# Optimization experiments

Measured on AMD Instinct MI355X. Metric: run time of the kernel, lower is better.

## Reference

```python
import jax, jax.numpy as jnp
import numpy as np
from jax import lax

B, C, T = 64, 122, 500
COUT, D, H, FF, L = 64, 128, 8, 256, 2
NSUB, NCLS = 13, 4
EPS = 1e-5


def _gelu(x):
    return jax.nn.gelu(x, approximate=False)  # torch nn.GELU default (erf)


def _bn(x, g, b, m, v):
    # eval-mode BatchNorm1d over channel dim of [N, C, T]
    scale = (g / jnp.sqrt(v + EPS))[None, :, None]
    return (x - m[None, :, None]) * scale + b[None, :, None]


def _ln(x, g, b):
    mu = x.mean(-1, keepdims=True)
    var = ((x - mu) ** 2).mean(-1, keepdims=True)
    return (x - mu) / jnp.sqrt(var + EPS) * g + b


def _conv1d(x, w, b, pad):
    y = lax.conv_general_dilated(x, w, (1,), [(pad, pad)], dimension_numbers=('NCH', 'OIH', 'NCH'))
    return y + b[None, :, None]


def forward(x, subject_ids, conv1_w, conv1_b, bn1_g, bn1_b, bn1_m, bn1_v,
            conv2_w, conv2_b, bn2_g, bn2_b, bn2_m, bn2_v,
            proj_w, proj_b, elec_emb,
            qkv_w, qkv_b, out_w, out_b, ln1_g, ln1_b,
            ff1_w, ff1_b, ff2_w, ff2_b, ln2_g, ln2_b,
            heads_w, heads_b):
    bsz = x.shape[0]
    h = x.reshape(bsz * C, 1, T)                               # [B*C, 1, T]
    h = _gelu(_bn(_conv1d(h, conv1_w, conv1_b, 4), bn1_g, bn1_b, bn1_m, bn1_v))
    h = h.reshape(bsz * C, COUT, T // 2, 2).max(-1)            # MaxPool1d(2)
    h = _gelu(_bn(_conv1d(h, conv2_w, conv2_b, 2), bn2_g, bn2_b, bn2_m, bn2_v))
    h = h.mean(-1)                                             # AdaptiveAvgPool1d(1)
    tok = h @ proj_w.T + proj_b                                # [B*C, D]
    tok = tok.reshape(bsz, C, D) + elec_emb[:, :C, :]
    dh = D // H
    inv_sqrt_dh = 1.0 / float(np.sqrt(dh))
    for l in range(L):  # post-norm TransformerEncoderLayer, gelu activation
        qkv = jnp.einsum('bsd,ed->bse', tok, qkv_w[l]) + qkv_b[l]
        q, k, v = jnp.split(qkv, 3, axis=-1)
        q = q.reshape(bsz, C, H, dh)
        k = k.reshape(bsz, C, H, dh)
        v = v.reshape(bsz, C, H, dh)
        att = jax.nn.softmax(jnp.einsum('bqhd,bkhd->bhqk', q, k) * inv_sqrt_dh, axis=-1)
        ctx = jnp.einsum('bhqk,bkhd->bqhd', att, v).reshape(bsz, C, D)
        tok = _ln(tok + ctx @ out_w[l].T + out_b[l], ln1_g[l], ln1_b[l])
        ff = _gelu(tok @ ff1_w[l].T + ff1_b[l]) @ ff2_w[l].T + ff2_b[l]
        tok = _ln(tok + ff, ln2_g[l], ln2_b[l])
    pooled = tok.mean(axis=1)                                  # [B, D]
    # per-subject head routing == gather subject's weight/bias, batched matvec
    hw = heads_w[subject_ids]                                  # [B, NCLS, D]
    hb = heads_b[subject_ids]                                  # [B, NCLS]
    return jnp.einsum('bd,bcd->bc', pooled, hw) + hb


def setup_inputs() -> dict:
    key = jax.random.key(0)
    ks = jax.random.split(key, 16)
    def n(i, shape, s=0.02):
        return jax.random.normal(ks[i], shape, jnp.float32) * s
    return {
        'x': jax.random.normal(ks[0], (B, C, T), jnp.float32),
        'subject_ids': jax.random.randint(ks[1], (B,), 0, NSUB),
        'conv1_w': n(2, (COUT, 1, 9), 0.3), 'conv1_b': jnp.zeros((COUT,), jnp.float32),
        'bn1_g': jnp.ones((COUT,), jnp.float32), 'bn1_b': jnp.zeros((COUT,), jnp.float32),
        'bn1_m': jnp.zeros((COUT,), jnp.float32), 'bn1_v': jnp.ones((COUT,), jnp.float32),
        'conv2_w': n(3, (COUT, COUT, 5), 0.05), 'conv2_b': jnp.zeros((COUT,), jnp.float32),
        'bn2_g': jnp.ones((COUT,), jnp.float32), 'bn2_b': jnp.zeros((COUT,), jnp.float32),
        'bn2_m': jnp.zeros((COUT,), jnp.float32), 'bn2_v': jnp.ones((COUT,), jnp.float32),
        'proj_w': n(4, (D, COUT), 0.05), 'proj_b': jnp.zeros((D,), jnp.float32),
        'elec_emb': n(5, (1, C, D), 0.02),
        'qkv_w': n(6, (L, 3 * D, D), 0.05), 'qkv_b': jnp.zeros((L, 3 * D), jnp.float32),
        'out_w': n(7, (L, D, D), 0.05), 'out_b': jnp.zeros((L, D), jnp.float32),
        'ln1_g': jnp.ones((L, D), jnp.float32), 'ln1_b': jnp.zeros((L, D), jnp.float32),
        'ff1_w': n(8, (L, FF, D), 0.05), 'ff1_b': jnp.zeros((L, FF), jnp.float32),
        'ff2_w': n(9, (L, D, FF), 0.05), 'ff2_b': jnp.zeros((L, D), jnp.float32),
        'ln2_g': jnp.ones((L, D), jnp.float32), 'ln2_b': jnp.zeros((L, D), jnp.float32),
        'heads_w': n(10, (NSUB, NCLS, D), 0.05), 'heads_b': jnp.zeros((NSUB, NCLS), jnp.float32),
    }


def reference(x, subject_ids, conv1_w, conv1_b, bn1_g, bn1_b, bn1_m, bn1_v,
              conv2_w, conv2_b, bn2_g, bn2_b, bn2_m, bn2_v,
              proj_w, proj_b, elec_emb,
              qkv_w, qkv_b, out_w, out_b, ln1_g, ln1_b,
              ff1_w, ff1_b, ff2_w, ff2_b, ln2_g, ln2_b,
              heads_w, heads_b):
    return forward(x, subject_ids, conv1_w, conv1_b, bn1_g, bn1_b, bn1_m, bn1_v,
                   conv2_w, conv2_b, bn2_g, bn2_b, bn2_m, bn2_v,
                   proj_w, proj_b, elec_emb,
                   qkv_w, qkv_b, out_w, out_b, ln1_g, ln1_b,
                   ff1_w, ff1_b, ff2_w, ff2_b, ln2_g, ln2_b,
                   heads_w, heads_b)
```

## Files before the change

### kernel.cpp

```cpp
#include <hip/hip_runtime.h>
#include <math.h>

#define BB 64
#define CC 122
#define TT 500
#define NCOUT 64
#define DD 128
#define HHEADS 8
#define FFDIM 256
#define NLAYER 2
#define EPS 1e-5f
#define SEQ (BB*CC)

#define WS_W2T     0u
#define WS_S1      20480u
#define WS_SH1     20544u
#define WS_S2      20608u
#define WS_SH2     20672u
#define WS_WBF     20736u
#define WS_TOK     151808u
#define WS_QKVB    1151232u
#define WS_VTB     2150656u
#define WS_GTAB    2674944u
#define WS_W1S     2675968u

#define WB_QKV  0u
#define WB_OUT  98304u
#define WB_FF1  131072u
#define WB_FF2  196608u

typedef __attribute__((ext_vector_type(8))) short bf16x8;
typedef __attribute__((ext_vector_type(4))) float f32x4;

__device__ __forceinline__ unsigned short f2bf(float f) {
    unsigned int u = __float_as_uint(f);
    unsigned int r = u + 0x7FFFu + ((u >> 16) & 1u);
    return (unsigned short)(r >> 16);
}

__device__ __forceinline__ float gelu_fast(float x) {
    float z = fabsf(x) * 0.70710678118654752f;
    float t = __builtin_amdgcn_rcpf(fmaf(0.3275911f, z, 1.0f));
    float p = fmaf(fmaf(fmaf(fmaf(1.061405429f, t, -1.453152027f), t,
                             1.421413741f), t, -0.284496736f), t, 0.254829592f);
    float e = __expf(-z * z);
    float erf_abs = fmaf(-p * t, e, 1.0f);
    float erf_x = copysignf(erf_abs, x);
    return 0.5f * x * (1.0f + erf_x);
}

__device__ __forceinline__ float gelu_tab(float x, const float* __restrict__ gt) {
    float p = fmaf(x, 32.0f, 256.0f);
    p = fminf(fmaxf(p, 0.0f), 511.999f);
    int i = (int)p;
    float fr = p - (float)i;
    float2 gd = *(const float2*)&gt[2*i];
    return fmaf(fr, gd.y, gd.x);
}

__global__ void prep_kernel(const float* __restrict__ conv1_w, const float* __restrict__ conv1_b,
                            const float* __restrict__ bn1_g, const float* __restrict__ bn1_b,
                            const float* __restrict__ bn1_m, const float* __restrict__ bn1_v,
                            const float* __restrict__ conv2_w, const float* __restrict__ conv2_b,
                            const float* __restrict__ bn2_g, const float* __restrict__ bn2_b,
                            const float* __restrict__ bn2_m, const float* __restrict__ bn2_v,
                            const float* __restrict__ qkv_w, const float* __restrict__ out_w,
                            const float* __restrict__ ff1_w, const float* __restrict__ ff2_w,
                            float* __restrict__ ws) {
    int idx = blockIdx.x * blockDim.x + threadIdx.x;
    if (idx < 20480) {
        int ci = idx & 63; int co = (idx >> 6) & 63; int kk = idx >> 12;
        unsigned short* wt = (unsigned short*)(ws + WS_W2T);
        wt[idx] = f2bf(conv2_w[(co*64 + ci)*5 + kk]);
    } else if (idx < 20544) {
        int i = idx - 20480;
        float s = bn1_g[i] * rsqrtf(bn1_v[i] + EPS);
        ws[WS_S1 + i] = s;
        ws[WS_SH1 + i] = (conv1_b[i] - bn1_m[i]) * s + bn1_b[i];
    } else if (idx < 20608) {
        int i = idx - 20544;
        float s = bn2_g[i] * rsqrtf(bn2_v[i] + EPS);
        ws[WS_S2 + i] = s;
        ws[WS_SH2 + i] = (conv2_b[i] - bn2_m[i]) * s + bn2_b[i];
    } else if (idx < 282752) {
        int r = idx - 20608;
        unsigned short* wbf = (unsigned short*)(ws + WS_WBF);
        float v;
        if (r < 98304)       v = qkv_w[r];
        else if (r < 131072) v = out_w[r - 98304];
        else if (r < 196608) v = ff1_w[r - 131072];
        else                 v = ff2_w[r - 196608];
        wbf[r] = f2bf(v);
    } else if (idx < 283264) {
        int i = idx - 282752;
        float x0 = (i - 256) * 0.03125f;
        float x1 = x0 + 0.03125f;
        float g0 = 0.5f*x0*(1.0f + erff(x0*0.70710678118654752f));
        float g1 = 0.5f*x1*(1.0f + erff(x1*0.70710678118654752f));
        ws[WS_GTAB + 2*i]     = g0;
        ws[WS_GTAB + 2*i + 1] = g1 - g0;
    } else if (idx < 285312) {
        int i = idx - 283264;
        int co = i >> 5, k = i & 31;
        unsigned short* w1s = (unsigned short*)(ws + WS_W1S);
        float s = bn1_g[co] * rsqrtf(bn1_v[co] + EPS);
        w1s[i] = (k < 9) ? f2bf(conv1_w[co*9 + k] * s) : (unsigned short)0;
    }
}

__global__ __launch_bounds__(256, 4) void conv_kernel(const float* __restrict__ x,
            const float* __restrict__ proj_w, const float* __restrict__ proj_b,
            const float* __restrict__ elec,
            const float* __restrict__ wsr, float* __restrict__ tok) {
    __shared__ __align__(16) unsigned short h1s[264*64];
    __shared__ __align__(16) unsigned short xbf[544];
    __shared__ __align__(16) float gtab[1024];
    __shared__ float part[256];
    __shared__ float mean_l[64];
    int n = blockIdx.x;
    int c = n % CC;
    int tid = threadIdx.x;
    const float* xg = x + (size_t)n * TT;

    for (int i = tid; i < 544; i += 256) {
        unsigned short v = 0;
        if (i >= 4 && i < 504) v = f2bf(xg[i-4]);
        xbf[i] = v;
    }
    {
        const float4* gsrc = (const float4*)(wsr + WS_GTAB);
        float4* gdst = (float4*)gtab;
        if (tid < 256) gdst[tid] = gsrc[tid];
    }
    for (int idx = tid; idx < 14*64; idx += 256) {
        int rr = idx >> 6;
        int r = (rr < 2) ? rr : (rr - 2 + 252);
        h1s[r*64 + (idx & 63)] = 0;
    }
    __syncthreads();

    int lane = tid & 63;
    int w = tid >> 6;
    int ln15 = lane & 15, lg = lane >> 4;

    {
        const unsigned short* w1s = (const unsigned short*)(wsr + WS_W1S);
        bf16x8 b1f[4];
        float sh1v[4];
#pragma unroll
        for (int nt = 0; nt < 4; nt++) {
            int co = nt*16 + ln15;
            b1f[nt] = *(const bf16x8*)&w1s[co*32 + lg*8];
            sh1v[nt] = wsr[WS_SH1 + co];
        }
        for (int mi = 0; mi < 8; mi++) {
            int mt = w*8 + mi;
            int t = mt*16 + ln15;
            short e[8];
#pragma unroll
            for (int j = 0; j < 8; j++) e[j] = (short)xbf[t + lg*8 + j];
            bf16x8 af = {e[0],e[1],e[2],e[3],e[4],e[5],e[6],e[7]};
#pragma unroll
            for (int nt = 0; nt < 4; nt++) {
                f32x4 cacc = __builtin_amdgcn_mfma_f32_16x16x32_bf16(af, b1f[nt],
                                (f32x4){0.f,0.f,0.f,0.f}, 0, 0, 0);
                float g0 = gelu_tab(cacc[0] + sh1v[nt], gtab);
                float g1 = gelu_tab(cacc[1] + sh1v[nt], gtab);
                float g2 = gelu_tab(cacc[2] + sh1v[nt], gtab);
                float g3 = gelu_tab(cacc[3] + sh1v[nt], gtab);
                int tpA = mt*8 + lg*2;
                if (tpA < 250) {
                    int co = nt*16 + ln15;
                    int r = tpA + 2;
                    int cp = (co >> 3) ^ (r & 7);
                    h1s[r*64 + cp*8 + (co & 7)] = f2bf(fmaxf(g0, g1));
                    int r2 = r + 1;
                    int cp2 = (co >> 3) ^ (r2 & 7);
                    h1s[r2*64 + cp2*8 + (co & 7)] = f2bf(fmaxf(g2, g3));
                }
            }
        }
    }
    __syncthreads();

    const unsigned short* wt = (const unsigned short*)(wsr + WS_W2T);
    f32x4 acc[4][4];
#pragma unroll
    for (int mi = 0; mi < 4; mi++)
#pragma unroll
        for (int nt = 0; nt < 4; nt++) acc[mi][nt] = (f32x4){0.f, 0.f, 0.f, 0.f};

    const unsigned short* wbase = wt + ln15*64 + lg*8;
#pragma unroll
    for (int kk = 0; kk < 5; kk++) {
#pragma unroll
        for (int s = 0; s < 2; s++) {
            bf16x8 bfv[4];
#pragma unroll
            for (int nt = 0; nt < 4; nt++)
                bfv[nt] = *(const bf16x8*)(wbase + kk*4096 + nt*1024 + s*32);
#pragma unroll
            for (int mi = 0; mi < 4; mi++) {
                int r = (w*4 + mi)*16 + ln15 + kk;
                int cp = (s*4 + lg) ^ (r & 7);
                bf16x8 af = *(const bf16x8*)&h1s[r*64 + cp*8];
#pragma unroll
                for (int nt = 0; nt < 4; nt++)
                    acc[mi][nt] = __builtin_amdgcn_mfma_f32_16x16x32_bf16(af, bfv[nt], acc[mi][nt], 0, 0, 0);
            }
        }
    }

#pragma unroll
    for (int nt = 0; nt < 4; nt++) {
        int co2 = nt*16 + ln15;
        float sc = wsr[WS_S2 + co2], sh = wsr[WS_SH2 + co2];
        float p = 0.f;
#pragma unroll
        for (int mi = 0; mi < 4; mi++) {
            int tbase = (w*4 + mi)*16 + lg*4;
#pragma unroll
            for (int i = 0; i < 4; i++) {
                if (tbase + i < 250)
                    p += gelu_tab(fmaf(acc[mi][nt][i], sc, sh), gtab);
            }
        }
        p += __shfl_down(p, 32, 64);
        p += __shfl_down(p, 16, 64);
        if (lane < 16) part[w*64 + co2] = p;
    }
    __syncthreads();
    if (tid < 64) {
        mean_l[tid] = (part[tid] + part[64+tid] + part[128+tid] + part[192+tid]) * (1.0f/250.0f);
    }
    __syncthreads();

    if (tid < DD) {
        int d = tid;
        float a = proj_b[d] + elec[c*DD + d];
#pragma unroll 8
        for (int o = 0; o < 64; o++) a = fmaf(mean_l[o], proj_w[d*64 + o], a);
        tok[(size_t)n * DD + d] = a;
    }
}

__global__ __launch_bounds__(256) void qkv_gemm(const float* __restrict__ Aptr,
        const unsigned short* __restrict__ Bbf,
        const float* __restrict__ bias,
        unsigned short* __restrict__ qkvb,
        unsigned short* __restrict__ vtb) {
    const int tid = threadIdx.x;
    const int m0 = blockIdx.x * 32;
    const int y  = blockIdx.y;
    const int n0 = y * 128;
    __shared__ __align__(16) unsigned short As[32*128];

    const float* A = Aptr + (size_t)m0 * 128;
    for (int i = tid; i < 1024; i += 256) {
        int m = i >> 5; int kq = (i & 31)*4;
        float4 v = *(const float4*)(A + m*128 + kq);
        int cp = (kq >> 3) ^ (m & 15);
        short4 s4 = make_short4((short)f2bf(v.x), (short)f2bf(v.y),
                                (short)f2bf(v.z), (short)f2bf(v.w));
        *(short4*)&As[m*128 + cp*8 + (kq & 7)] = s4;
    }
    __syncthreads();

    const int lane = tid & 63, w = tid >> 6;
    const int ln15 = lane & 15, lg = lane >> 4;
    f32x4 acc[2][2];
#pragma unroll
    for (int mi = 0; mi < 2; mi++)
#pragma unroll
        for (int ni = 0; ni < 2; ni++) acc[mi][ni] = (f32x4){0.f, 0.f, 0.f, 0.f};

    const unsigned short* Bb = Bbf + (size_t)n0 * 128;
#pragma unroll
    for (int kt = 0; kt < 4; kt++) {
        bf16x8 af[2], bfv[2];
#pragma unroll
        for (int mi = 0; mi < 2; mi++) {
            int m = mi*16 + ln15;
            int cp = (kt*4 + lg) ^ (m & 15);
            af[mi] = *(const bf16x8*)&As[m*128 + cp*8];
        }
#pragma unroll
        for (int ni = 0; ni < 2; ni++) {
            int nn = (w*2 + ni)*16 + ln15;
            bfv[ni] = *(const bf16x8*)&Bb[(size_t)nn*128 + kt*32 + lg*8];
        }
#pragma unroll
        for (int mi = 0; mi < 2; mi++)
#pragma unroll
            for (int ni = 0; ni < 2; ni++)
                acc[mi][ni] = __builtin_amdgcn_mfma_f32_16x16x32_bf16(af[mi], bfv[ni], acc[mi][ni], 0, 0, 0);
    }

#pragma unroll
    for (int mi = 0; mi < 2; mi++)
#pragma unroll
        for (int ni = 0; ni < 2; ni++) {
            int nloc = (w*2 + ni)*16 + ln15;
            float bb = bias[n0 + nloc];
#pragma unroll
            for (int i = 0; i < 4; i++) {
                int ml = mi*16 + lg*4 + i;
                int nrow = m0 + ml;
                unsigned short us = f2bf(acc[mi][ni][i] + bb);
                if (y < 2) {
                    qkvb[(size_t)nrow*256 + n0 + nloc] = us;
                } else {
                    int bq = nrow / 122;
                    int j  = nrow - bq*122;
                    vtb[((size_t)(bq*128 + nloc))*128 + j] = us;
                }
            }
        }
}

__global__ __launch_bounds__(256) void attn_tail(
        const unsigned short* __restrict__ qkvb,
        const unsigned short* __restrict__ vtb,
        const unsigned short* __restrict__ outW, const float* __restrict__ outb,
        float* __restrict__ tok,
        const float* __restrict__ ln1g, const float* __restrict__ ln1b,
        const unsigned short* __restrict__ B1, const float* __restrict__ b1,
        const unsigned short* __restrict__ B2, const float* __restrict__ b2,
        const float* __restrict__ ln2g, const float* __restrict__ ln2b) {
    __shared__ float Cs[32*129];
    __shared__ __align__(16) unsigned short Pregion[4*32*128];
    __shared__ __align__(16) unsigned short ctxs[32*128];

    const int tid = threadIdx.x;
    const int blk = blockIdx.x;
    const int b = blk >> 2, mq = blk & 3;
    const int m0l = mq * 32;
    const int lane = tid & 63, w = tid >> 6;
    const int ln15 = lane & 15, lg = lane >> 4;

    const unsigned short* qb = qkvb + (size_t)b * 122 * 256;
    unsigned short* Pw = Pregion + w * 4096;

#pragma unroll
    for (int hs = 0; hs < 2; hs++) {
        int h = w + hs*4;
        bf16x8 af[2];
#pragma unroll
        for (int mi = 0; mi < 2; mi++) {
            int mrow = m0l + mi*16 + ln15;
            int gr = (mrow < 122) ? mrow : 121;
            bf16x8 z = {0,0,0,0,0,0,0,0};
            if (lg < 2) z = *(const bf16x8*)(qb + gr*256 + h*16 + lg*8);
            af[mi] = z;
        }
        f32x4 S[2][8];
#pragma unroll
        for (int nt = 0; nt < 8; nt++) {
            int j = nt*16 + ln15;
            int gj = (j < 122) ? j : 121;
            bf16x8 bv = {0,0,0,0,0,0,0,0};
            if (lg < 2) bv = *(const bf16x8*)(qb + gj*256 + 128 + h*16 + lg*8);
#pragma unroll
            for (int mi = 0; mi < 2; mi++)
                S[mi][nt] = __builtin_amdgcn_mfma_f32_16x16x32_bf16(af[mi], bv,
                                (f32x4){0.f,0.f,0.f,0.f}, 0, 0, 0);
        }
        float sm[2][4];
#pragma unroll
        for (int mi = 0; mi < 2; mi++)
#pragma unroll
            for (int i = 0; i < 4; i++) {
                float m_ = -1e30f;
#pragma unroll
                for (int nt = 0; nt < 8; nt++) {
                    float v = S[mi][nt][i] * 0.25f;
                    if (nt == 7 && ln15 >= 10) v = -1e30f;
                    S[mi][nt][i] = v;
                    m_ = fmaxf(m_, v);
                }
                m_ = fmaxf(m_, __shfl_xor(m_, 1, 64));
                m_ = fmaxf(m_, __shfl_xor(m_, 2, 64));
                m_ = fmaxf(m_, __shfl_xor(m_, 4, 64));
                m_ = fmaxf(m_, __shfl_xor(m_, 8, 64));
                float s_ = 0.f;
#pragma unroll
                for (int nt = 0; nt < 8; nt++) {
                    float e = __expf(S[mi][nt][i] - m_);
                    S[mi][nt][i] = e;
                    s_ += e;
                }
                s_ += __shfl_xor(s_, 1, 64);
                s_ += __shfl_xor(s_, 2, 64);
                s_ += __shfl_xor(s_, 4, 64);
                s_ += __shfl_xor(s_, 8, 64);
                sm[mi][i] = s_;
            }
#pragma unroll
        for (int mi = 0; mi < 2; mi++)
#pragma unroll
            for (int nt = 0; nt < 8; nt++)
#pragma unroll
                for (int i = 0; i < 4; i++) {
                    int rp = mi*16 + lg*4 + i;
                    int j = nt*16 + ln15;
                    int cp = (j >> 3) ^ (rp & 15);
                    Pw[rp*128 + cp*8 + (j & 7)] = f2bf(S[mi][nt][i]);
                }
        f32x4 cacc[2] = {(f32x4){0.f,0.f,0.f,0.f}, (f32x4){0.f,0.f,0.f,0.f}};
#pragma unroll
        for (int kt = 0; kt < 4; kt++) {
            bf16x8 bv = *(const bf16x8*)(vtb + ((size_t)(b*128 + h*16 + ln15))*128 + kt*32 + lg*8);
#pragma unroll
            for (int mi = 0; mi < 2; mi++) {
                int m = mi*16 + ln15;
                int cp = (kt*4 + lg) ^ (m & 15);
                bf16x8 ap = *(const bf16x8*)&Pw[m*128 + cp*8];
                cacc[mi] = __builtin_amdgcn_mfma_f32_16x16x32_bf16(ap, bv, cacc[mi], 0, 0, 0);
            }
        }
#pragma unroll
        for (int mi = 0; mi < 2; mi++)
#pragma unroll
            for (int i = 0; i < 4; i++) {
                float inv = __builtin_amdgcn_rcpf(sm[mi][i]);
                int rp = mi*16 + lg*4 + i;
                int ccol = h*16 + ln15;
                int cp = (ccol >> 3) ^ (rp & 15);
                ctxs[rp*128 + cp*8 + (ccol & 7)] = f2bf(cacc[mi][i] * inv);
            }
    }
    __syncthreads();

    {
        f32x4 acc[2][2];
#pragma unroll
        for (int mi = 0; mi < 2; mi++)
#pragma unroll
            for (int ni = 0; ni < 2; ni++) acc[mi][ni] = (f32x4){0.f,0.f,0.f,0.f};
#pragma unroll
        for (int kt = 0; kt < 4; kt++) {
            bf16x8 afm[2], bv[2];
#pragma unroll
            for (int mi = 0; mi < 2; mi++) {
                int m = mi*16 + ln15;
                int cp = (kt*4 + lg) ^ (m & 15);
                afm[mi] = *(const bf16x8*)&ctxs[m*128 + cp*8];
            }
#pragma unroll
            for (int ni = 0; ni < 2; ni++) {
                int nn = (w*2 + ni)*16 + ln15;
                bv[ni] = *(const bf16x8*)&outW[(size_t)nn*128 + kt*32 + lg*8];
            }
#pragma unroll
            for (int mi = 0; mi < 2; mi++)
#pragma unroll
                for (int ni = 0; ni < 2; ni++)
                    acc[mi][ni] = __builtin_amdgcn_mfma_f32_16x16x32_bf16(afm[mi], bv[ni], acc[mi][ni], 0, 0, 0);
        }
#pragma unroll
        for (int mi = 0; mi < 2; mi++)
#pragma unroll
            for (int ni = 0; ni < 2; ni++) {
                int nloc = (w*2 + ni)*16 + ln15;
                float bb = outb[nloc];
#pragma unroll
                for (int i = 0; i < 4; i++) {
                    int ml = mi*16 + lg*4 + i;
                    int mrow = m0l + ml;
                    int grow = b*122 + ((mrow < 122) ? mrow : 121);
                    Cs[ml*129 + nloc] = acc[mi][ni][i] + bb + tok[(size_t)grow*128 + nloc];
                }
            }
    }
    __syncthreads();

    unsigned short* ln1buf = Pregion;
    unsigned short* Hs = Pregion + 4096;
    {
        int r = tid >> 3, sub = tid & 7;
        float s1 = 0.f, s2 = 0.f;
#pragma unroll
        for (int j = 0; j < 16; j++) {
            float vv = Cs[r*129 + sub*16 + j];
            s1 += vv; s2 += vv*vv;
        }
        s1 += __shfl_down(s1, 4, 64); s2 += __shfl_down(s2, 4, 64);
        s1 += __shfl_down(s1, 2, 64); s2 += __shfl_down(s2, 2, 64);
        s1 += __shfl_down(s1, 1, 64); s2 += __shfl_down(s2, 1, 64);
        int lb = lane & 56;
        s1 = __shfl(s1, lb, 64); s2 = __shfl(s2, lb, 64);
        float mu = s1 * (1.0f/128.0f);
        float var = s2 * (1.0f/128.0f) - mu*mu;
        float rstd = rsqrtf(var + EPS);
#pragma unroll
        for (int j = 0; j < 16; j++) {
            int nloc = sub*16 + j;
            float vv = (Cs[r*129 + nloc] - mu) * rstd * ln1g[nloc] + ln1b[nloc];
            Cs[r*129 + nloc] = vv;
            int cp = (nloc >> 3) ^ (r & 15);
            ln1buf[r*128 + cp*8 + (nloc & 7)] = f2bf(vv);
        }
    }
    __syncthreads();

    {
        f32x4 acc1[2][4];
#pragma unroll
        for (int mi = 0; mi < 2; mi++)
#pragma unroll
            for (int ni = 0; ni < 4; ni++) acc1[mi][ni] = (f32x4){0.f,0.f,0.f,0.f};
#pragma unroll
        for (int kt = 0; kt < 4; kt++) {
            bf16x8 afm[2];
#pragma unroll
            for (int mi = 0; mi < 2; mi++) {
                int m = mi*16 + ln15;
                int cp = (kt*4 + lg) ^ (m & 15);
                afm[mi] = *(const bf16x8*)&ln1buf[m*128 + cp*8];
            }
#pragma unroll
            for (int ni = 0; ni < 4; ni++) {
                int nn = w*64 + ni*16 + ln15;
                bf16x8 bv = *(const bf16x8*)&B1[(size_t)nn*128 + kt*32 + lg*8];
#pragma unroll
                for (int mi = 0; mi < 2; mi++)
                    acc1[mi][ni] = __builtin_amdgcn_mfma_f32_16x16x32_bf16(afm[mi], bv, acc1[mi][ni], 0, 0, 0);
            }
        }
#pragma unroll
        for (int ni = 0; ni < 4; ni++) {
            int nn = w*64 + ni*16 + ln15;
            float bb = b1[nn];
#pragma unroll
            for (int mi = 0; mi < 2; mi++)
#pragma unroll
                for (int i = 0; i < 4; i++) {
                    int m = mi*16 + lg*4 + i;
                    float v = gelu_fast(acc1[mi][ni][i] + bb);
                    int cp = (nn >> 3) ^ (m & 15);
                    Hs[m*256 + cp*8 + (nn & 7)] = f2bf(v);
                }
        }
    }
    __syncthreads();

    {
        f32x4 acc2[2][2];
#pragma unroll
        for (int mi = 0; mi < 2; mi++)
#pragma unroll
            for (int ni = 0; ni < 2; ni++) acc2[mi][ni] = (f32x4){0.f,0.f,0.f,0.f};
#pragma unroll
        for (int kt = 0; kt < 8; kt++) {
            bf16x8 afm[2];
#pragma unroll
            for (int mi = 0; mi < 2; mi++) {
                int m = mi*16 + ln15;
                int cp = (kt*4 + lg) ^ (m & 15);
                afm[mi] = *(const bf16x8*)&Hs[m*256 + cp*8];
            }
#pragma unroll
            for (int ni = 0; ni < 2; ni++) {
                int nn = (w*2 + ni)*16 + ln15;
                bf16x8 bv = *(const bf16x8*)&B2[(size_t)nn*256 + kt*32 + lg*8];
#pragma unroll
                for (int mi = 0; mi < 2; mi++)
                    acc2[mi][ni] = __builtin_amdgcn_mfma_f32_16x16x32_bf16(afm[mi], bv, acc2[mi][ni], 0, 0, 0);
            }
        }
#pragma unroll
        for (int mi = 0; mi < 2; mi++)
#pragma unroll
            for (int ni = 0; ni < 2; ni++) {
                int nloc = (w*2 + ni)*16 + ln15;
                float bb = b2[nloc];
#pragma unroll
                for (int i = 0; i < 4; i++) {
                    int ml = mi*16 + lg*4 + i;
                    Cs[ml*129 + nloc] = acc2[mi][ni][i] + bb + Cs[ml*129 + nloc];
                }
            }
    }
    __syncthreads();

    {
        int r = tid >> 3, sub = tid & 7;
        float s1 = 0.f, s2 = 0.f;
#pragma unroll
        for (int j = 0; j < 16; j++) {
            float vv = Cs[r*129 + sub*16 + j];
            s1 += vv; s2 += vv*vv;
        }
        s1 += __shfl_down(s1, 4, 64); s2 += __shfl_down(s2, 4, 64);
        s1 += __shfl_down(s1, 2, 64); s2 += __shfl_down(s2, 2, 64);
        s1 += __shfl_down(s1, 1, 64); s2 += __shfl_down(s2, 1, 64);
        int lb = lane & 56;
        s1 = __shfl(s1, lb, 64); s2 = __shfl(s2, lb, 64);
        float mu = s1 * (1.0f/128.0f);
        float var = s2 * (1.0f/128.0f) - mu*mu;
        float rstd = rsqrtf(var + EPS);
        if (m0l + r < 122) {
#pragma unroll
            for (int j = 0; j < 16; j++) {
                int nloc = sub*16 + j;
                float vv = (Cs[r*129 + nloc] - mu) * rstd * ln2g[nloc] + ln2b[nloc];
                tok[((size_t)(b*122 + m0l + r))*128 + nloc] = vv;
            }
        }
    }
}

__global__ __launch_bounds__(128) void final_kernel(const float* __restrict__ tok,
        const int* __restrict__ sid,
        const float* __restrict__ hw, const float* __restrict__ hb,
        float* __restrict__ outp) {
    __shared__ float pool[DD];
    int b = blockIdx.x, tid = threadIdx.x;
    float s = 0.f;
    for (int c2 = 0; c2 < CC; c2++) s += tok[((size_t)b*CC + c2)*DD + tid];
    pool[tid] = s * (1.0f/(float)CC);
    __syncthreads();
    if (tid < 4) {
        int sb = sid[b];
        const float* w = hw + ((size_t)sb*4 + tid)*DD;
        float a = hb[sb*4 + tid];
#pragma unroll 8
        for (int d = 0; d < DD; d++) a = fmaf(pool[d], w[d], a);
        outp[b*4 + tid] = a;
    }
}

extern "C" void kernel_launch(void* const* d_in, const int* in_sizes, int n_in,
                              void* d_out, int out_size, void* d_ws, size_t ws_size,
                              hipStream_t stream) {
    const float* x       = (const float*)d_in[0];
    const int*   sid     = (const int*)  d_in[1];
    const float* conv1_w = (const float*)d_in[2];
    const float* conv1_b = (const float*)d_in[3];
    const float* bn1_g   = (const float*)d_in[4];
    const float* bn1_b   = (const float*)d_in[5];
    const float* bn1_m   = (const float*)d_in[6];
    const float* bn1_v   = (const float*)d_in[7];
    const float* conv2_w = (const float*)d_in[8];
    const float* conv2_b = (const float*)d_in[9];
    const float* bn2_g   = (const float*)d_in[10];
    const float* bn2_b   = (const float*)d_in[11];
    const float* bn2_m   = (const float*)d_in[12];
    const float* bn2_v   = (const float*)d_in[13];
    const float* proj_w  = (const float*)d_in[14];
    const float* proj_b  = (const float*)d_in[15];
    const float* elec    = (const float*)d_in[16];
    const float* qkv_w   = (const float*)d_in[17];
    const float* qkv_b   = (const float*)d_in[18];
    const float* out_w   = (const float*)d_in[19];
    const float* out_b   = (const float*)d_in[20];
    const float* ln1_g   = (const float*)d_in[21];
    const float* ln1_b   = (const float*)d_in[22];
    const float* ff1_w   = (const float*)d_in[23];
    const float* ff1_b   = (const float*)d_in[24];
    const float* ff2_w   = (const float*)d_in[25];
    const float* ff2_b   = (const float*)d_in[26];
    const float* ln2_g   = (const float*)d_in[27];
    const float* ln2_b   = (const float*)d_in[28];
    const float* heads_w = (const float*)d_in[29];
    const float* heads_b = (const float*)d_in[30];
    float* ws = (float*)d_ws;
    const unsigned short* wbf = (const unsigned short*)(ws + WS_WBF);
    unsigned short* qkvb = (unsigned short*)(ws + WS_QKVB);
    unsigned short* vtb  = (unsigned short*)(ws + WS_VTB);

    prep_kernel<<<(285312 + 255)/256, 256, 0, stream>>>(
        conv1_w, conv1_b, bn1_g, bn1_b, bn1_m, bn1_v,
        conv2_w, conv2_b, bn2_g, bn2_b, bn2_m, bn2_v,
        qkv_w, out_w, ff1_w, ff2_w, ws);

    conv_kernel<<<SEQ, 256, 0, stream>>>(x, proj_w, proj_b, elec, ws, ws + WS_TOK);

    for (int l = 0; l < NLAYER; l++) {
        qkv_gemm<<<dim3(244,3), 256, 0, stream>>>(
            ws + WS_TOK, wbf + WB_QKV + l*49152, qkv_b + l*384, qkvb, vtb);
        attn_tail<<<BB*4, 256, 0, stream>>>(
            qkvb, vtb,
            wbf + WB_OUT + l*16384, out_b + l*128,
            ws + WS_TOK, ln1_g + l*128, ln1_b + l*128,
            wbf + WB_FF1 + l*32768, ff1_b + l*256,
            wbf + WB_FF2 + l*32768, ff2_b + l*128,
            ln2_g + l*128, ln2_b + l*128);
    }

    final_kernel<<<BB, 128, 0, stream>>>(ws + WS_TOK, sid, heads_w, heads_b, (float*)d_out);
}
```

Baseline: 434.5 us.

## Double attn_tail block to 512 threads, one wave per head

The attention/FFN tail kernel goes from 4 to 8 waves per block. Each wave now handles one head instead of two, and the out-proj, FF1, FF2 and layernorm phases are re-split across 8 waves with smaller per-wave tiles. The aim is more latency hiding and more parallel work, since the grid has only 256 blocks. In exchange, the per-wave P buffer shrinks to 16 rows, so each wave processes its two 16-row M tiles one after the other, and there are more barrier participants.

```diff
diff --git a/kernel.cpp b/kernel.cpp
--- a/kernel.cpp
+++ b/kernel.cpp
@@ -318,7 +318,7 @@
         }
 }
 
-__global__ __launch_bounds__(256) void attn_tail(
+__global__ __launch_bounds__(512) void attn_tail(
         const unsigned short* __restrict__ qkvb,
         const unsigned short* __restrict__ vtb,
         const unsigned short* __restrict__ outW, const float* __restrict__ outb,
@@ -328,7 +328,7 @@
         const unsigned short* __restrict__ B2, const float* __restrict__ b2,
         const float* __restrict__ ln2g, const float* __restrict__ ln2b) {
     __shared__ float Cs[32*129];
-    __shared__ __align__(16) unsigned short Pregion[4*32*128];
+    __shared__ __align__(16) unsigned short Pregion[8*16*128];
     __shared__ __align__(16) unsigned short ctxs[32*128];
 
     const int tid = threadIdx.x;
@@ -339,43 +339,35 @@
     const int ln15 = lane & 15, lg = lane >> 4;
 
     const unsigned short* qb = qkvb + (size_t)b * 122 * 256;
-    unsigned short* Pw = Pregion + w * 4096;
-
-#pragma unroll
-    for (int hs = 0; hs < 2; hs++) {
-        int h = w + hs*4;
-        bf16x8 af[2];
-#pragma unroll
-        for (int mi = 0; mi < 2; mi++) {
-            int mrow = m0l + mi*16 + ln15;
+    unsigned short* Pw = Pregion + w * 2048;
+
+    {
+        const int h = w;
+#pragma unroll
+        for (int mt = 0; mt < 2; mt++) {
+            int mrow = m0l + mt*16 + ln15;
             int gr = (mrow < 122) ? mrow : 121;
-            bf16x8 z = {0,0,0,0,0,0,0,0};
-            if (lg < 2) z = *(const bf16x8*)(qb + gr*256 + h*16 + lg*8);
-            af[mi] = z;
-        }
-        f32x4 S[2][8];
-#pragma unroll
-        for (int nt = 0; nt < 8; nt++) {
-            int j = nt*16 + ln15;
-            int gj = (j < 122) ? j : 121;
-            bf16x8 bv = {0,0,0,0,0,0,0,0};
-            if (lg < 2) bv = *(const bf16x8*)(qb + gj*256 + 128 + h*16 + lg*8);
-#pragma unroll
-            for (int mi = 0; mi < 2; mi++)
-                S[mi][nt] = __builtin_amdgcn_mfma_f32_16x16x32_bf16(af[mi], bv,
-                                (f32x4){0.f,0.f,0.f,0.f}, 0, 0, 0);
-        }
-        float sm[2][4];
-#pragma unroll
-        for (int mi = 0; mi < 2; mi++)
+            bf16x8 af = {0,0,0,0,0,0,0,0};
+            if (lg < 2) af = *(const bf16x8*)(qb + gr*256 + h*16 + lg*8);
+            f32x4 S[8];
+#pragma unroll
+            for (int nt = 0; nt < 8; nt++) {
+                int j = nt*16 + ln15;
+                int gj = (j < 122) ? j : 121;
+                bf16x8 bv = {0,0,0,0,0,0,0,0};
+                if (lg < 2) bv = *(const bf16x8*)(qb + gj*256 + 128 + h*16 + lg*8);
+                S[nt] = __builtin_amdgcn_mfma_f32_16x16x32_bf16(af, bv,
+                            (f32x4){0.f,0.f,0.f,0.f}, 0, 0, 0);
+            }
+            float sm[4];
 #pragma unroll
             for (int i = 0; i < 4; i++) {
                 float m_ = -1e30f;
 #pragma unroll
                 for (int nt = 0; nt < 8; nt++) {
-                    float v = S[mi][nt][i] * 0.25f;
+                    float v = S[nt][i] * 0.25f;
                     if (nt == 7 && ln15 >= 10) v = -1e30f;
-                    S[mi][nt][i] = v;
+                    S[nt][i] = v;
                     m_ = fmaxf(m_, v);
                 }
                 m_ = fmaxf(m_, __shfl_xor(m_, 1, 64));
@@ -385,91 +377,71 @@
                 float s_ = 0.f;
 #pragma unroll
                 for (int nt = 0; nt < 8; nt++) {
-                    float e = __expf(S[mi][nt][i] - m_);
-                    S[mi][nt][i] = e;
+                    float e = __expf(S[nt][i] - m_);
+                    S[nt][i] = e;
                     s_ += e;
                 }
                 s_ += __shfl_xor(s_, 1, 64);
                 s_ += __shfl_xor(s_, 2, 64);
                 s_ += __shfl_xor(s_, 4, 64);
                 s_ += __shfl_xor(s_, 8, 64);
-                sm[mi][i] = s_;
-            }
-#pragma unroll
-        for (int mi = 0; mi < 2; mi++)
+                sm[i] = s_;
+            }
 #pragma unroll
             for (int nt = 0; nt < 8; nt++)
 #pragma unroll
                 for (int i = 0; i < 4; i++) {
-                    int rp = mi*16 + lg*4 + i;
+                    int rp = lg*4 + i;
                     int j = nt*16 + ln15;
-                    int cp = (j >> 3) ^ (rp & 15);
-                    Pw[rp*128 + cp*8 + (j & 7)] = f2bf(S[mi][nt][i]);
+                    int cp = (j >> 3) ^ rp;
+                    Pw[rp*128 + cp*8 + (j & 7)] = f2bf(S[nt][i]);
                 }
-        f32x4 cacc[2] = {(f32x4){0.f,0.f,0.f,0.f}, (f32x4){0.f,0.f,0.f,0.f}};
+            f32x4 cacc = (f32x4){0.f,0.f,0.f,0.f};
+#pragma unroll
+            for (int kt = 0; kt < 4; kt++) {
+                bf16x8 bv = *(const bf16x8*)(vtb + ((size_t)(b*128 + h*16 + ln15))*128 + kt*32 + lg*8);
+                int m = ln15;
+                int cp = (kt*4 + lg) ^ m;
+                bf16x8 ap = *(const bf16x8*)&Pw[m*128 + cp*8];
+                cacc = __builtin_amdgcn_mfma_f32_16x16x32_bf16(ap, bv, cacc, 0, 0, 0);
+            }
+#pragma unroll
+            for (int i = 0; i < 4; i++) {
+                float inv = __builtin_amdgcn_rcpf(sm[i]);
+                int rp = mt*16 + lg*4 + i;
+                int ccol = h*16 + ln15;
+                int cp = (ccol >> 3) ^ (rp & 15);
+                ctxs[rp*128 + cp*8 + (ccol & 7)] = f2bf(cacc[i] * inv);
+            }
+        }
+    }
+    __syncthreads();
+
+    {
+        f32x4 acc[2];
+#pragma unroll
+        for (int mi = 0; mi < 2; mi++) acc[mi] = (f32x4){0.f,0.f,0.f,0.f};
+        int nn = w*16 + ln15;
 #pragma unroll
         for (int kt = 0; kt < 4; kt++) {
-            bf16x8 bv = *(const bf16x8*)(vtb + ((size_t)(b*128 + h*16 + ln15))*128 + kt*32 + lg*8);
+            bf16x8 bv = *(const bf16x8*)&outW[(size_t)nn*128 + kt*32 + lg*8];
 #pragma unroll
             for (int mi = 0; mi < 2; mi++) {
                 int m = mi*16 + ln15;
                 int cp = (kt*4 + lg) ^ (m & 15);
-                bf16x8 ap = *(const bf16x8*)&Pw[m*128 + cp*8];
-                cacc[mi] = __builtin_amdgcn_mfma_f32_16x16x32_bf16(ap, bv, cacc[mi], 0, 0, 0);
-            }
-        }
+                bf16x8 afm = *(const bf16x8*)&ctxs[m*128 + cp*8];
+                acc[mi] = __builtin_amdgcn_mfma_f32_16x16x32_bf16(afm, bv, acc[mi], 0, 0, 0);
+            }
+        }
+        float bb = outb[nn];
 #pragma unroll
         for (int mi = 0; mi < 2; mi++)
 #pragma unroll
             for (int i = 0; i < 4; i++) {
-                float inv = __builtin_amdgcn_rcpf(sm[mi][i]);
-                int rp = mi*16 + lg*4 + i;
-                int ccol = h*16 + ln15;
-                int cp = (ccol >> 3) ^ (rp & 15);
-                ctxs[rp*128 + cp*8 + (ccol & 7)] = f2bf(cacc[mi][i] * inv);
-            }
-    }
-    __syncthreads();
-
-    {
-        f32x4 acc[2][2];
-#pragma unroll
-        for (int mi = 0; mi < 2; mi++)
-#pragma unroll
-            for (int ni = 0; ni < 2; ni++) acc[mi][ni] = (f32x4){0.f,0.f,0.f,0.f};
-#pragma unroll
-        for (int kt = 0; kt < 4; kt++) {
-            bf16x8 afm[2], bv[2];
-#pragma unroll
-            for (int mi = 0; mi < 2; mi++) {
-                int m = mi*16 + ln15;
-                int cp = (kt*4 + lg) ^ (m & 15);
-                afm[mi] = *(const bf16x8*)&ctxs[m*128 + cp*8];
-            }
-#pragma unroll
-            for (int ni = 0; ni < 2; ni++) {
-                int nn = (w*2 + ni)*16 + ln15;
-                bv[ni] = *(const bf16x8*)&outW[(size_t)nn*128 + kt*32 + lg*8];
-            }
-#pragma unroll
-            for (int mi = 0; mi < 2; mi++)
-#pragma unroll
-                for (int ni = 0; ni < 2; ni++)
-                    acc[mi][ni] = __builtin_amdgcn_mfma_f32_16x16x32_bf16(afm[mi], bv[ni], acc[mi][ni], 0, 0, 0);
-        }
-#pragma unroll
-        for (int mi = 0; mi < 2; mi++)
-#pragma unroll
-            for (int ni = 0; ni < 2; ni++) {
-                int nloc = (w*2 + ni)*16 + ln15;
-                float bb = outb[nloc];
-#pragma unroll
-                for (int i = 0; i < 4; i++) {
-                    int ml = mi*16 + lg*4 + i;
-                    int mrow = m0l + ml;
-                    int grow = b*122 + ((mrow < 122) ? mrow : 121);
-                    Cs[ml*129 + nloc] = acc[mi][ni][i] + bb + tok[(size_t)grow*128 + nloc];
-                }
+                int ml = mi*16 + lg*4 + i;
+                int mrow = m0l + ml;
+                int grow = b*122 + ((mrow < 122) ? mrow : 121);
+                Cs[ml*129 + nn] = acc[mi][i] + bb + tok[(size_t)grow*128 + nn];
             }
     }
     __syncthreads();
@@ -477,24 +449,23 @@
     unsigned short* ln1buf = Pregion;
     unsigned short* Hs = Pregion + 4096;
     {
-        int r = tid >> 3, sub = tid & 7;
+        int r = tid >> 4, sub = tid & 15;
         float s1 = 0.f, s2 = 0.f;
 #pragma unroll
-        for (int j = 0; j < 16; j++) {
-            float vv = Cs[r*129 + sub*16 + j];
+        for (int j = 0; j < 8; j++) {
+            float vv = Cs[r*129 + sub*8 + j];
             s1 += vv; s2 += vv*vv;
         }
-        s1 += __shfl_down(s1, 4, 64); s2 += __shfl_down(s2, 4, 64);
-        s1 += __shfl_down(s1, 2, 64); s2 += __shfl_down(s2, 2, 64);
-        s1 += __shfl_down(s1, 1, 64); s2 += __shfl_down(s2, 1, 64);
-        int lb = lane & 56;
-        s1 = __shfl(s1, lb, 64); s2 = __shfl(s2, lb, 64);
+        s1 += __shfl_xor(s1, 1, 64); s2 += __shfl_xor(s2, 1, 64);
+        s1 += __shfl_xor(s1, 2, 64); s2 += __shfl_xor(s2, 2, 64);
+        s1 += __shfl_xor(s1, 4, 64); s2 += __shfl_xor(s2, 4, 64);
+        s1 += __shfl_xor(s1, 8, 64); s2 += __shfl_xor(s2, 8, 64);
         float mu = s1 * (1.0f/128.0f);
         float var = s2 * (1.0f/128.0f) - mu*mu;
         float rstd = rsqrtf(var + EPS);
 #pragma unroll
-        for (int j = 0; j < 16; j++) {
-            int nloc = sub*16 + j;
+        for (int j = 0; j < 8; j++) {
+            int nloc = sub*8 + j;
             float vv = (Cs[r*129 + nloc] - mu) * rstd * ln1g[nloc] + ln1b[nloc];
             Cs[r*129 + nloc] = vv;
             int cp = (nloc >> 3) ^ (r & 15);
@@ -504,11 +475,11 @@
     __syncthreads();
 
     {
-        f32x4 acc1[2][4];
+        f32x4 acc1[2][2];
 #pragma unroll
         for (int mi = 0; mi < 2; mi++)
 #pragma unroll
-            for (int ni = 0; ni < 4; ni++) acc1[mi][ni] = (f32x4){0.f,0.f,0.f,0.f};
+            for (int ni = 0; ni < 2; ni++) acc1[mi][ni] = (f32x4){0.f,0.f,0.f,0.f};
 #pragma unroll
         for (int kt = 0; kt < 4; kt++) {
             bf16x8 afm[2];
@@ -519,8 +490,8 @@
                 afm[mi] = *(const bf16x8*)&ln1buf[m*128 + cp*8];
             }
 #pragma unroll
-            for (int ni = 0; ni < 4; ni++) {
-                int nn = w*64 + ni*16 + ln15;
+            for (int ni = 0; ni < 2; ni++) {
+                int nn = (w*2 + ni)*16 + ln15;
                 bf16x8 bv = *(const bf16x8*)&B1[(size_t)nn*128 + kt*32 + lg*8];
 #pragma unroll
                 for (int mi = 0; mi < 2; mi++)
@@ -528,8 +499,8 @@
             }
         }
 #pragma unroll
-        for (int ni = 0; ni < 4; ni++) {
-            int nn = w*64 + ni*16 + ln15;
+        for (int ni = 0; ni < 2; ni++) {
+            int nn = (w*2 + ni)*16 + ln15;
             float bb = b1[nn];
 #pragma unroll
             for (int mi = 0; mi < 2; mi++)
@@ -545,64 +516,51 @@
     __syncthreads();
 
     {
-        f32x4 acc2[2][2];
-#pragma unroll
-        for (int mi = 0; mi < 2; mi++)
-#pragma unroll
-            for (int ni = 0; ni < 2; ni++) acc2[mi][ni] = (f32x4){0.f,0.f,0.f,0.f};
+        f32x4 acc2[2];
+#pragma unroll
+        for (int mi = 0; mi < 2; mi++) acc2[mi] = (f32x4){0.f,0.f,0.f,0.f};
+        int nn = w*16 + ln15;
 #pragma unroll
         for (int kt = 0; kt < 8; kt++) {
-            bf16x8 afm[2];
+            bf16x8 bv = *(const bf16x8*)&B2[(size_t)nn*256 + kt*32 + lg*8];
 #pragma unroll
             for (int mi = 0; mi < 2; mi++) {
                 int m = mi*16 + ln15;
                 int cp = (kt*4 + lg) ^ (m & 15);
-                afm[mi] = *(const bf16x8*)&Hs[m*256 + cp*8];
-            }
-#pragma unroll
-            for (int ni = 0; ni < 2; ni++) {
-                int nn = (w*2 + ni)*16 + ln15;
-                bf16x8 bv = *(const bf16x8*)&B2[(size_t)nn*256 + kt*32 + lg*8];
-#pragma unroll
-                for (int mi = 0; mi < 2; mi++)
-                    acc2[mi][ni] = __builtin_amdgcn_mfma_f32_16x16x32_bf16(afm[mi], bv, acc2[mi][ni], 0, 0, 0);
-            }
-        }
+                bf16x8 afm = *(const bf16x8*)&Hs[m*256 + cp*8];
+                acc2[mi] = __builtin_amdgcn_mfma_f32_16x16x32_bf16(afm, bv, acc2[mi], 0, 0, 0);
+            }
+        }
+        float bb = b2[nn];
 #pragma unroll
         for (int mi = 0; mi < 2; mi++)
 #pragma unroll
-            for (int ni = 0; ni < 2; ni++) {
-                int nloc = (w*2 + ni)*16 + ln15;
-                float bb = b2[nloc];
-#pragma unroll
-                for (int i = 0; i < 4; i++) {
-                    int ml = mi*16 + lg*4 + i;
-                    Cs[ml*129 + nloc] = acc2[mi][ni][i] + bb + Cs[ml*129 + nloc];
-                }
-            }
-    }
-    __syncthreads();
-
-    {
-        int r = tid >> 3, sub = tid & 7;
+            for (int i = 0; i < 4; i++) {
+                int ml = mi*16 + lg*4 + i;
+                Cs[ml*129 + nn] = acc2[mi][i] + bb + Cs[ml*129 + nn];
+            }
+    }
+    __syncthreads();
+
+    {
+        int r = tid >> 4, sub = tid & 15;
         float s1 = 0.f, s2 = 0.f;
 #pragma unroll
-        for (int j = 0; j < 16; j++) {
-            float vv = Cs[r*129 + sub*16 + j];
+        for (int j = 0; j < 8; j++) {
+            float vv = Cs[r*129 + sub*8 + j];
             s1 += vv; s2 += vv*vv;
         }
-        s1 += __shfl_down(s1, 4, 64); s2 += __shfl_down(s2, 4, 64);
-        s1 += __shfl_down(s1, 2, 64); s2 += __shfl_down(s2, 2, 64);
-        s1 += __shfl_down(s1, 1, 64); s2 += __shfl_down(s2, 1, 64);
-        int lb = lane & 56;
-        s1 = __shfl(s1, lb, 64); s2 = __shfl(s2, lb, 64);
+        s1 += __shfl_xor(s1, 1, 64); s2 += __shfl_xor(s2, 1, 64);
+        s1 += __shfl_xor(s1, 2, 64); s2 += __shfl_xor(s2, 2, 64);
+        s1 += __shfl_xor(s1, 4, 64); s2 += __shfl_xor(s2, 4, 64);
+        s1 += __shfl_xor(s1, 8, 64); s2 += __shfl_xor(s2, 8, 64);
         float mu = s1 * (1.0f/128.0f);
         float var = s2 * (1.0f/128.0f) - mu*mu;
         float rstd = rsqrtf(var + EPS);
         if (m0l + r < 122) {
 #pragma unroll
-            for (int j = 0; j < 16; j++) {
-                int nloc = sub*16 + j;
+            for (int j = 0; j < 8; j++) {
+                int nloc = sub*8 + j;
                 float vv = (Cs[r*129 + nloc] - mu) * rstd * ln2g[nloc] + ln2b[nloc];
                 tok[((size_t)(b*122 + m0l + r))*128 + nloc] = vv;
             }
@@ -679,7 +637,7 @@
     for (int l = 0; l < NLAYER; l++) {
         qkv_gemm<<<dim3(244,3), 256, 0, stream>>>(
             ws + WS_TOK, wbf + WB_QKV + l*49152, qkv_b + l*384, qkvb, vtb);
-        attn_tail<<<BB*4, 256, 0, stream>>>(
+        attn_tail<<<BB*4, 512, 0, stream>>>(
             qkvb, vtb,
             wbf + WB_OUT + l*16384, out_b + l*128,
             ws + WS_TOK, ln1_g + l*128, ln1_b + l*128,
```

Result: no change. 429.3 us (-1.2%).
